# Optimization experiments

Measured on AMD Instinct MI355X. Metric: run time of the kernel, lower is better.

Reference implementation:

```python
import jax, jax.numpy as jnp
import numpy as np

N, M, D = 8192, 8192, 256
GAMMA = 1.0 / D  # standard RBF bandwidth gamma = 1/D


def setup_inputs() -> dict:
    key = jax.random.key(0)
    kx, ks = jax.random.split(key)
    x = jax.random.normal(kx, (N, D), dtype=jnp.float32)
    support = jax.random.normal(ks, (M, D), dtype=jnp.float32)
    return {"x": x, "support": support}


def reference(x, support):
    # Vectorized RBF Gram matrix: K[i, j] = exp(-gamma * ||x_i - s_j||^2)
    # ||x_i - s_j||^2 = ||x_i||^2 + ||s_j||^2 - 2 x_i . s_j  (cdist-style, one GEMM)
    x_sq = jnp.sum(x * x, axis=-1, keepdims=True)            # [N, 1]
    s_sq = jnp.sum(support * support, axis=-1)[None, :]      # [1, M]
    cross = jnp.einsum('nd,md->nm', x, support)              # [N, M]
    sq_dists = jnp.maximum(x_sq + s_sq - 2.0 * cross, 0.0)   # clamp fp error
    return jnp.exp(-GAMMA * sq_dists)
```

## Files before the change

### kernel.cpp

```cpp
#include <hip/hip_runtime.h>

#define N 8192
#define M 8192
#define D 256

typedef unsigned short ushort_t;
typedef __attribute__((ext_vector_type(8))) short short8;
typedef __attribute__((ext_vector_type(4))) float floatx4;

__device__ __forceinline__ unsigned short f2bf(float f) {
  unsigned int u = __float_as_uint(f);
  u += 0x7fffu + ((u >> 16) & 1u);
  return (unsigned short)(u >> 16);
}

__global__ __launch_bounds__(256) void prep_kernel(const float* __restrict__ x,
                                                   const float* __restrict__ s,
                                                   ushort_t* __restrict__ xb,
                                                   ushort_t* __restrict__ sb,
                                                   float* __restrict__ xn,
                                                   float* __restrict__ sn) {
  int gw = blockIdx.x * 4 + (threadIdx.x >> 6);
  int lane = threadIdx.x & 63;
  const float* src;
  ushort_t* dst;
  float* nrm;
  int row;
  if (gw < N) { src = x; dst = xb; nrm = xn; row = gw; }
  else        { src = s; dst = sb; nrm = sn; row = gw - N; }
  float4 v = ((const float4*)(src + (size_t)row * D))[lane];
  float ss = v.x * v.x + v.y * v.y + v.z * v.z + v.w * v.w;
  ushort4 o;
  o.x = f2bf(v.x); o.y = f2bf(v.y); o.z = f2bf(v.z); o.w = f2bf(v.w);
  int lr = row & 127;
  size_t off = (size_t)(row >> 7) * 65536 + (size_t)(lane >> 4) * 16384
             + (size_t)lr * 128
             + (size_t)(((((lane >> 1) & 7) ^ (lr & 7)) * 16) + (lane & 1) * 8);
  *(ushort4*)((char*)dst + off) = o;
#pragma unroll
  for (int offs = 32; offs > 0; offs >>= 1) ss += __shfl_down(ss, offs);
  if (lane == 0) nrm[row] = ss;
}

__device__ __forceinline__ void compute_round(const ushort_t* __restrict__ As,
                                              const ushort_t* __restrict__ Bs,
                                              floatx4 (&acc)[4][4], int wr, int wc,
                                              int q4, int m16) {
#pragma unroll
  for (int cc = 0; cc < 2; ++cc) {
    short8 a_frag[4], b_frag[4];
#pragma unroll
    for (int i = 0; i < 4; ++i) {
      const int row = wr + i * 16 + m16;
      a_frag[i] = *(const short8*)(As + row * 64 + (((cc * 4 + q4) ^ (row & 7)) << 3));
    }
#pragma unroll
    for (int j = 0; j < 4; ++j) {
      const int row = wc + j * 16 + m16;
      b_frag[j] = *(const short8*)(Bs + row * 64 + (((cc * 4 + q4) ^ (row & 7)) << 3));
    }
#pragma unroll
    for (int i = 0; i < 4; ++i)
#pragma unroll
      for (int j = 0; j < 4; ++j)
        acc[i][j] = __builtin_amdgcn_mfma_f32_16x16x32_bf16(a_frag[i], b_frag[j],
                                                            acc[i][j], 0, 0, 0);
  }
}

__device__ __forceinline__ void stage_round(const char* gA, const char* gB,
                                            char* lA, char* lB) {
#pragma unroll
  for (int i = 0; i < 4; ++i)
    __builtin_amdgcn_global_load_lds(
        (const __attribute__((address_space(1))) void*)(gA + i * 1024),
        (__attribute__((address_space(3))) void*)(lA + i * 1024), 16, 0, 0);
#pragma unroll
  for (int i = 0; i < 4; ++i)
    __builtin_amdgcn_global_load_lds(
        (const __attribute__((address_space(1))) void*)(gB + i * 1024),
        (__attribute__((address_space(3))) void*)(lB + i * 1024), 16, 0, 0);
}

__global__ __launch_bounds__(256, 3) void rbf_gemm(const ushort_t* __restrict__ X,
                                                   const ushort_t* __restrict__ S,
                                                   const float* __restrict__ xn,
                                                   const float* __restrict__ sn,
                                                   float* __restrict__ out) {
  __shared__ __attribute__((aligned(16))) ushort_t As[128 * 64];
  __shared__ __attribute__((aligned(16))) ushort_t Bs[128 * 64];
  __shared__ float nS[256];

  const int tid = threadIdx.x;
  const int lane = tid & 63;
  const int wave = tid >> 6;
  const int bx = blockIdx.x;
  const int by = blockIdx.y;

  {
    const float* np = (tid < 128) ? (xn + by * 128 + tid)
                                  : (sn + bx * 128 + (tid - 128));
    nS[tid] = *np;
  }

  const char* gA = (const char*)X + (size_t)by * 65536 + wave * 4096 + lane * 16;
  const char* gB = (const char*)S + (size_t)bx * 65536 + wave * 4096 + lane * 16;
  char* lA = (char*)As + wave * 4096;
  char* lB = (char*)Bs + wave * 4096;

  const int wr = (wave >> 1) * 64;
  const int wc = (wave & 1) * 64;
  const int q4 = lane >> 4;
  const int m16 = lane & 15;

  floatx4 acc[4][4];
#pragma unroll
  for (int i = 0; i < 4; ++i)
#pragma unroll
    for (int j = 0; j < 4; ++j) acc[i][j] = (floatx4){0.f, 0.f, 0.f, 0.f};

#pragma unroll
  for (int r = 0; r < 4; ++r) {
    __syncthreads();
    stage_round(gA + r * 16384, gB + r * 16384, lA, lB);
    __syncthreads();
    compute_round(As, Bs, acc, wr, wc, q4, m16);
  }

  const float cexp = -1.0f / (float)D;
#pragma unroll
  for (int i = 0; i < 4; ++i) {
#pragma unroll
    for (int j = 0; j < 4; ++j) {
#pragma unroll
      for (int r = 0; r < 4; ++r) {
        const int rl = wr + i * 16 + q4 * 4 + r;
        const int cl = wc + j * 16 + m16;
        float sq = nS[rl] + nS[128 + cl] - 2.0f * acc[i][j][r];
        sq = fmaxf(sq, 0.0f);
        __builtin_nontemporal_store(
            __expf(cexp * sq),
            out + (size_t)(by * 128 + rl) * M + (bx * 128 + cl));
      }
    }
  }
}

extern "C" void kernel_launch(void* const* d_in, const int* in_sizes, int n_in,
                              void* d_out, int out_size, void* d_ws, size_t ws_size,
                              hipStream_t stream) {
  const float* x = (const float*)d_in[0];
  const float* s = (const float*)d_in[1];
  float* out = (float*)d_out;
  char* ws = (char*)d_ws;
  ushort_t* xb = (ushort_t*)ws;
  ushort_t* sb = (ushort_t*)(ws + (size_t)N * D * 2);
  float* xn = (float*)(ws + (size_t)(N + M) * D * 2);
  float* sn = xn + N;

  prep_kernel<<<(N + M) / 4, 256, 0, stream>>>(x, s, xb, sb, xn, sn);
  dim3 grid(M / 128, N / 128);
  rbf_gemm<<<grid, 256, 0, stream>>>(xb, sb, xn, sn, out);
}
```

Before: 302.8 us.

## Load MFMA fragments directly from global in pre-packed layout, drop LDS staging

The prep kernel now writes bf16 operands in a fragment-major layout, so each wave can load its MFMA A/B fragments straight from global memory with contiguous 16-byte loads. The GEMM drops LDS staging and the per-round barriers, and adds a grouped block-index swizzle meant to improve L2 reuse. The goal is to remove LDS traffic and synchronisation. The cost is that operand data is read redundantly by the two waves sharing each row or column block, relying on cache hits instead of on-chip sharing.

```diff
diff --git a/kernel.cpp b/kernel.cpp
--- a/kernel.cpp
+++ b/kernel.cpp
@@ -32,54 +32,17 @@
   float ss = v.x * v.x + v.y * v.y + v.z * v.z + v.w * v.w;
   ushort4 o;
   o.x = f2bf(v.x); o.y = f2bf(v.y); o.z = f2bf(v.z); o.w = f2bf(v.w);
-  int lr = row & 127;
-  size_t off = (size_t)(row >> 7) * 65536 + (size_t)(lane >> 4) * 16384
-             + (size_t)lr * 128
-             + (size_t)(((((lane >> 1) & 7) ^ (lr & 7)) * 16) + (lane & 1) * 8);
+  const int g = row >> 6;
+  const int sub = (row >> 4) & 3;
+  const int m = row & 15;
+  const int c = lane >> 3;
+  const int q = (lane >> 1) & 3;
+  size_t off = (size_t)g * 32768 +
+               (size_t)((c * 4 + sub) * 1024 + q * 256 + m * 16 + (lane & 1) * 8);
   *(ushort4*)((char*)dst + off) = o;
 #pragma unroll
   for (int offs = 32; offs > 0; offs >>= 1) ss += __shfl_down(ss, offs);
   if (lane == 0) nrm[row] = ss;
-}
-
-__device__ __forceinline__ void compute_round(const ushort_t* __restrict__ As,
-                                              const ushort_t* __restrict__ Bs,
-                                              floatx4 (&acc)[4][4], int wr, int wc,
-                                              int q4, int m16) {
-#pragma unroll
-  for (int cc = 0; cc < 2; ++cc) {
-    short8 a_frag[4], b_frag[4];
-#pragma unroll
-    for (int i = 0; i < 4; ++i) {
-      const int row = wr + i * 16 + m16;
-      a_frag[i] = *(const short8*)(As + row * 64 + (((cc * 4 + q4) ^ (row & 7)) << 3));
-    }
-#pragma unroll
-    for (int j = 0; j < 4; ++j) {
-      const int row = wc + j * 16 + m16;
-      b_frag[j] = *(const short8*)(Bs + row * 64 + (((cc * 4 + q4) ^ (row & 7)) << 3));
-    }
-#pragma unroll
-    for (int i = 0; i < 4; ++i)
-#pragma unroll
-      for (int j = 0; j < 4; ++j)
-        acc[i][j] = __builtin_amdgcn_mfma_f32_16x16x32_bf16(a_frag[i], b_frag[j],
-                                                            acc[i][j], 0, 0, 0);
-  }
-}
-
-__device__ __forceinline__ void stage_round(const char* gA, const char* gB,
-                                            char* lA, char* lB) {
-#pragma unroll
-  for (int i = 0; i < 4; ++i)
-    __builtin_amdgcn_global_load_lds(
-        (const __attribute__((address_space(1))) void*)(gA + i * 1024),
-        (__attribute__((address_space(3))) void*)(lA + i * 1024), 16, 0, 0);
-#pragma unroll
-  for (int i = 0; i < 4; ++i)
-    __builtin_amdgcn_global_load_lds(
-        (const __attribute__((address_space(1))) void*)(gB + i * 1024),
-        (__attribute__((address_space(3))) void*)(lB + i * 1024), 16, 0, 0);
 }
 
 __global__ __launch_bounds__(256, 3) void rbf_gemm(const ushort_t* __restrict__ X,
@@ -87,31 +50,22 @@
                                                    const float* __restrict__ xn,
                                                    const float* __restrict__ sn,
                                                    float* __restrict__ out) {
-  __shared__ __attribute__((aligned(16))) ushort_t As[128 * 64];
-  __shared__ __attribute__((aligned(16))) ushort_t Bs[128 * 64];
   __shared__ float nS[256];
 
   const int tid = threadIdx.x;
   const int lane = tid & 63;
   const int wave = tid >> 6;
-  const int bx = blockIdx.x;
-  const int by = blockIdx.y;
 
-  {
-    const float* np = (tid < 128) ? (xn + by * 128 + tid)
-                                  : (sn + bx * 128 + (tid - 128));
-    nS[tid] = *np;
-  }
+  const int wg = blockIdx.y * 64 + blockIdx.x;
+  const int swz = (wg & 7) * 512 + (wg >> 3);
+  const int by = swz >> 6;
+  const int bx = swz & 63;
 
-  const char* gA = (const char*)X + (size_t)by * 65536 + wave * 4096 + lane * 16;
-  const char* gB = (const char*)S + (size_t)bx * 65536 + wave * 4096 + lane * 16;
-  char* lA = (char*)As + wave * 4096;
-  char* lB = (char*)Bs + wave * 4096;
+  if (tid < 128) nS[tid] = xn[by * 128 + tid];
+  else           nS[tid - 128 + 128] = sn[bx * 128 + (tid - 128)];
 
-  const int wr = (wave >> 1) * 64;
-  const int wc = (wave & 1) * 64;
-  const int q4 = lane >> 4;
-  const int m16 = lane & 15;
+  const char* aw = (const char*)X + (size_t)(by * 2 + (wave >> 1)) * 32768 + lane * 16;
+  const char* bw = (const char*)S + (size_t)(bx * 2 + (wave & 1)) * 32768 + lane * 16;
 
   floatx4 acc[4][4];
 #pragma unroll
@@ -120,13 +74,28 @@
     for (int j = 0; j < 4; ++j) acc[i][j] = (floatx4){0.f, 0.f, 0.f, 0.f};
 
 #pragma unroll
-  for (int r = 0; r < 4; ++r) {
-    __syncthreads();
-    stage_round(gA + r * 16384, gB + r * 16384, lA, lB);
-    __syncthreads();
-    compute_round(As, Bs, acc, wr, wc, q4, m16);
+  for (int c = 0; c < 8; ++c) {
+    short8 af[4], bf[4];
+#pragma unroll
+    for (int i = 0; i < 4; ++i)
+      af[i] = *(const short8*)(aw + (c * 4 + i) * 1024);
+#pragma unroll
+    for (int j = 0; j < 4; ++j)
+      bf[j] = *(const short8*)(bw + (c * 4 + j) * 1024);
+#pragma unroll
+    for (int i = 0; i < 4; ++i)
+#pragma unroll
+      for (int j = 0; j < 4; ++j)
+        acc[i][j] = __builtin_amdgcn_mfma_f32_16x16x32_bf16(af[i], bf[j],
+                                                            acc[i][j], 0, 0, 0);
   }
 
+  __syncthreads();
+
+  const int wr = (wave >> 1) * 64;
+  const int wc = (wave & 1) * 64;
+  const int q4 = lane >> 4;
+  const int m16 = lane & 15;
   const float cexp = -1.0f / (float)D;
 #pragma unroll
   for (int i = 0; i < 4; ++i) {
```

After: 325.3 us. +7.4%, slower.
